# Kernel tuning notes

Measured on AMD Instinct MI355X. Metric: run time of the kernel, lower is better.

## Reference

```python
import jax, jax.numpy as jnp
import numpy as np

NEG_SLOPE = 0.01  # torch LeakyReLU default
VAR = 0.1


def _leaky(z):
    return jnp.where(z >= 0, z, NEG_SLOPE * z)


def _sconv(theta, bias, L, x):
    # theta: (C_out, C_in, 2), L: (M, M), x: (B, C_in, M)
    Lx = jnp.einsum('mn,bin->bim', L, x)                     # degree-1 Laplacian term
    y = jnp.einsum('oi,bim->bom', theta[:, :, 0], x) \
        + jnp.einsum('oi,bim->bom', theta[:, :, 1], Lx)
    if bias is not None:
        y = y + bias
    return y


def setup_inputs() -> dict:
    key = jax.random.key(0)
    ks = iter(jax.random.split(key, 32))
    B, Cin = 8, 4
    Ms = [2000, 6000, 4000]
    inp = {}
    for d, M in enumerate(Ms):
        inp[f'L{d}'] = jax.random.normal(next(ks), (M, M), jnp.float32) / np.sqrt(M)
        inp[f'x{d}'] = jax.random.normal(next(ks), (B, Cin, M), jnp.float32)
        inp[f'th{d}_1'] = VAR * jax.random.normal(next(ks), (16, 4, 2), jnp.float32)
        inp[f'b{d}_1'] = jnp.zeros((1, 16, 1), jnp.float32)
        inp[f'th{d}_2'] = VAR * jax.random.normal(next(ks), (32, 16, 2), jnp.float32)
    dims = [(96, 64), (64, 32), (32, 16), (16, 2)]
    for i, (din, dout) in enumerate(dims, start=1):
        bound = 1.0 / np.sqrt(din)
        inp[f'W{i}'] = jax.random.uniform(next(ks), (dout, din), jnp.float32, -bound, bound)
        inp[f'bb{i}'] = jax.random.uniform(next(ks), (dout,), jnp.float32, -bound, bound)
    return inp


def reference(L0, L1, L2, x0, x1, x2,
              th0_1, b0_1, th0_2,
              th1_1, b1_1, th1_2,
              th2_1, b2_1, th2_2,
              W1, bb1, W2, bb2, W3, bb3, W4, bb4):
    out0_1 = _sconv(th0_1, b0_1, L0, x0)
    out1_1 = _sconv(th1_1, b1_1, L1, x1)
    out2_1 = _sconv(th2_1, b2_1, L2, x2)
    out0_2 = _sconv(th0_2, None, L0, _leaky(out0_1))   # (B, 32, M0)
    out1_2 = _sconv(th1_2, None, L1, _leaky(out1_1))
    out2_2 = _sconv(th2_2, None, L2, _leaky(out2_1))
    # mean-pool over simplices, concat along channel dim -> (B, 96)
    pooled = jnp.concatenate([out0_2.mean(axis=2), out1_2.mean(axis=2), out2_2.mean(axis=2)], axis=1)
    h = pooled @ W1.T + bb1      # dropouts are identity at inference
    h = h @ W2.T + bb2
    h = h @ W3.T + bb3
    logits = h @ W4.T + bb4      # (B, 2)
    return (logits, out0_2, out1_2, out2_2)
```

## Files before the change

kernel.cpp:

```cpp
#include <hip/hip_runtime.h>
#include <stdint.h>

typedef __attribute__((ext_vector_type(4))) float f32x4;
typedef __attribute__((ext_vector_type(8))) __bf16 bf16x8;

constexpr int MS_[3] = {2000, 6000, 4000};
constexpr int MP_[3] = {2048, 6016, 4032};
constexpr int KS_[3] = {512, 1536, 1024};
constexpr int RB_[3] = {32, 94, 63};
constexpr int NB_[3] = {128, 376, 252};
constexpr int NTILE = 189;
constexpr int NGEMMB = 756;
constexpr long long OUT_OFF_[3] = {16, 512016, 2048016};

__device__ __forceinline__ unsigned short f2bf(float f) {
  __bf16 b = (__bf16)f;
  return *reinterpret_cast<unsigned short*>(&b);
}

__device__ __forceinline__ void gload_lds16(const void* g, void* l) {
  __builtin_amdgcn_global_load_lds(
      (const __attribute__((address_space(1))) unsigned int*)g,
      (__attribute__((address_space(3))) unsigned int*)l, 16, 0, 0);
}

__device__ __forceinline__ void tile_decode(int bid, int& d, int& t) {
  if (bid < RB_[0]) { d = 0; t = bid; }
  else if (bid < RB_[0] + RB_[1]) { d = 1; t = bid - RB_[0]; }
  else { d = 2; t = bid - RB_[0] - RB_[1]; }
}

struct PrepArgs {
  const float* x[3];
  unsigned short* xT[3];
  float* zero0; int zero_n;
};

__global__ __launch_bounds__(256) void prep_k(PrepArgs pa) {
  int d, t; tile_decode(blockIdx.x, d, t);
  const int M = MS_[d], Mp = MP_[d];
  const float* x = pa.x[d];
  unsigned short* xT = pa.xT[d];
  const int tid = threadIdx.x;
  const int m0 = t * 64;
  const int ml = tid & 63, cg = tid >> 6;
  const int m = m0 + ml;
  const bool valid = m < M;
#pragma unroll
  for (int it = 0; it < 8; ++it) {
    int c = it * 4 + cg;
    float v = valid ? x[(size_t)c * M + m] : 0.f;
    xT[(size_t)c * Mp + m] = f2bf(v);
  }
  if (blockIdx.x == 0) {
    for (int i = tid; i < pa.zero_n; i += 256) pa.zero0[i] = 0.f;
  }
}

struct GemmArgs {
  const float* L[3];
  const unsigned short* B[3];
  float* P[3];
};

template <int BN>
__global__ __launch_bounds__(256) void gemm_k(GemmArgs ga) {
  const int bid = blockIdx.x;
  int d, local;
  if (bid < NB_[0]) { d = 0; local = bid; }
  else if (bid < NB_[0] + NB_[1]) { d = 1; local = bid - NB_[0]; }
  else { d = 2; local = bid - NB_[0] - NB_[1]; }

  int M, Mp, KS, r, s;
  if (d == 0) { M = MS_[0]; Mp = MP_[0]; KS = KS_[0]; r = local & 31; s = local >> 5; }
  else if (d == 1) { M = MS_[1]; Mp = MP_[1]; KS = KS_[1]; r = local % 94; s = local / 94; }
  else { M = MS_[2]; Mp = MP_[2]; KS = KS_[2]; r = local % 63; s = local / 63; }

  const float* Lp = ga.L[d];
  const unsigned short* Bt = ga.B[d];
  float* Pp = ga.P[d];

  const int m0 = r * 64;
  const int kt0 = s * KS;
  const int nsteps = KS >> 6;

  __shared__ __align__(16) unsigned short Al[2][64 * 64];
  __shared__ __align__(16) unsigned short Bl[2][BN * 64];

  const int tid = threadIdx.x;
  const int lane = tid & 63;
  const int wave = tid >> 6;
  const int wr = wave >> 1, wc = wave & 1;
  constexpr int NR = BN / 32;

  f32x4 acc[2][NR];
#pragma unroll
  for (int a = 0; a < 2; ++a)
#pragma unroll
    for (int b = 0; b < NR; ++b) acc[a][b] = (f32x4){0.f, 0.f, 0.f, 0.f};

  auto stage = [&](int buf, int kt) {
#pragma unroll
    for (int l2 = 0; l2 < 2; ++l2) {
      int q = l2 * 256 + tid;
      int row = q >> 3;
      int col8 = (q & 7) * 8;
      int gm = m0 + row, gk = kt + col8;
      float4 v0 = make_float4(0.f, 0.f, 0.f, 0.f), v1 = v0;
      if (gm < M && gk < M) {
        const float* p = Lp + (size_t)gm * M + gk;
        v0 = *reinterpret_cast<const float4*>(p);
        v1 = *reinterpret_cast<const float4*>(p + 4);
      }
      union { unsigned short u[8]; int4 v; } pk;
      pk.u[0] = f2bf(v0.x); pk.u[1] = f2bf(v0.y); pk.u[2] = f2bf(v0.z); pk.u[3] = f2bf(v0.w);
      pk.u[4] = f2bf(v1.x); pk.u[5] = f2bf(v1.y); pk.u[6] = f2bf(v1.z); pk.u[7] = f2bf(v1.w);
      int idx = (row * 64 + col8) ^ ((row & 7) << 3);
      *reinterpret_cast<int4*>(&Al[buf][idx]) = pk.v;
    }
    int kb = (kt + 64 <= Mp) ? kt : (Mp - 64);
#pragma unroll
    for (int is = 0; is < BN / 32; ++is) {
      int c = is * 32 + (tid >> 3);
      int ke = ((tid & 7) * 8) ^ ((c & 7) << 3);
      gload_lds16(Bt + (size_t)c * Mp + kb + ke, &Bl[buf][is * 2048 + tid * 8]);
    }
  };

  auto compute = [&](int buf) {
    bf16x8 af[2][2];
    const int rA = wr * 32 + (lane & 15);
    const int kl = (lane >> 4) * 8;
#pragma unroll
    for (int mr = 0; mr < 2; ++mr)
#pragma unroll
      for (int kk = 0; kk < 2; ++kk) {
        int rr = rA + mr * 16;
        int idx = (rr * 64 + kk * 32 + kl) ^ ((rr & 7) << 3);
        af[mr][kk] = *reinterpret_cast<const bf16x8*>(&Al[buf][idx]);
      }
    bf16x8 bfr[NR][2];
    const int cB = wc * (BN / 2) + (lane & 15);
#pragma unroll
    for (int nr = 0; nr < NR; ++nr)
#pragma unroll
      for (int kk = 0; kk < 2; ++kk) {
        int cc = cB + nr * 16;
        int idx = (cc * 64 + kk * 32 + kl) ^ ((cc & 7) << 3);
        bfr[nr][kk] = *reinterpret_cast<const bf16x8*>(&Bl[buf][idx]);
      }
#pragma unroll
    for (int kk = 0; kk < 2; ++kk)
#pragma unroll
      for (int mr = 0; mr < 2; ++mr)
#pragma unroll
        for (int nr = 0; nr < NR; ++nr)
          acc[mr][nr] = __builtin_amdgcn_mfma_f32_16x16x32_bf16(
              af[mr][kk], bfr[nr][kk], acc[mr][nr], 0, 0, 0);
  };

  stage(0, kt0);
  for (int t = 0; t < nsteps; ++t) {
    __syncthreads();
    if (t + 1 < nsteps) stage((t + 1) & 1, kt0 + (t + 1) * 64);
    compute(t & 1);
  }

  const int colb = wc * (BN / 2) + (lane & 15);
  const int rowb = m0 + wr * 32 + ((lane >> 4) << 2);
#pragma unroll
  for (int mr = 0; mr < 2; ++mr)
#pragma unroll
    for (int nr = 0; nr < NR; ++nr)
#pragma unroll
      for (int j = 0; j < 4; ++j) {
        int rr = rowb + mr * 16 + j;
        int cc = colb + nr * 16;
        Pp[((size_t)s * Mp + rr) * BN + cc] = acc[mr][nr][j];
      }
}

struct EpiAArgs {
  const float* part1[3];
  const float* x[3];
  const float* th1[3];
  const float* b1[3];
  unsigned short* zT[3];
};

__global__ __launch_bounds__(256) void epiA_k(EpiAArgs ea) {
  int d, t; tile_decode(blockIdx.x, d, t);
  const int M = MS_[d], Mp = MP_[d];
  const int m0 = t * 64;
  __shared__ float Ys[32 * 66];
  __shared__ float Xs[32 * 66];
  const int tid = threadIdx.x;
  const float* part = ea.part1[d];
#pragma unroll
  for (int it = 0; it < 8; ++it) {
    int idx = it * 256 + tid;
    int m = idx >> 5, c = idx & 31;
    size_t base = (size_t)(m0 + m) * 32 + c;
    size_t st = (size_t)Mp * 32;
    float ssum = part[base] + part[st + base] + part[2 * st + base] + part[3 * st + base];
    Ys[c * 66 + m] = ssum;
  }
  {
    const float* x = ea.x[d];
    int m = tid & 63, cg = tid >> 6;
    bool valid = (m0 + m) < M;
#pragma unroll
    for (int it = 0; it < 8; ++it) {
      int c = it * 4 + cg;
      Xs[c * 66 + m] = valid ? x[(size_t)c * M + m0 + m] : 0.f;
    }
  }
  __syncthreads();
  const float* th = ea.th1[d];
  const float* bias = ea.b1[d];
  unsigned short* zT = ea.zT[d];
  const int m = tid & 63, cog = tid >> 6;
  const bool valid = (m0 + m) < M;
#pragma unroll
  for (int it = 0; it < 32; ++it) {
    int co = it * 4 + cog;
    int o = co & 15, b = co >> 4;
    float a = bias[o];
#pragma unroll
    for (int i = 0; i < 4; ++i) {
      int ci = b * 4 + i;
      a += th[(o * 4 + i) * 2] * Xs[ci * 66 + m] + th[(o * 4 + i) * 2 + 1] * Ys[ci * 66 + m];
    }
    float zz = (a >= 0.f) ? a : 0.01f * a;
    zT[(size_t)co * Mp + m0 + m] = valid ? f2bf(zz) : (unsigned short)0;
  }
}

struct EpiBArgs {
  const float* part2[3];
  const unsigned short* zT[3];
  const float* th2[3];
  float* out;
  float* csz;
  float* csy;
};

__global__ __launch_bounds__(256) void epiB_k(EpiBArgs eb) {
  int d, t; tile_decode(blockIdx.x, d, t);
  const int M = MS_[d], Mp = MP_[d];
  const int m0 = t * 64;
  __shared__ float Ys[128 * 66];
  __shared__ float red[256];
  const int tid = threadIdx.x;
  const float* part = eb.part2[d];
  float csum = 0.f;
#pragma unroll
  for (int it = 0; it < 32; ++it) {
    int idx = it * 256 + tid;
    int m = idx >> 7, c = idx & 127;
    size_t base = (size_t)(m0 + m) * 128 + c;
    size_t st = (size_t)Mp * 128;
    float ssum = part[base] + part[st + base] + part[2 * st + base] + part[3 * st + base];
    Ys[c * 66 + m] = ssum;
    csum += ssum;
  }
  red[tid] = csum;
  __syncthreads();
  if (tid < 128) atomicAdd(&eb.csy[d * 128 + tid], red[tid] + red[tid + 128]);

  const unsigned short* zT = eb.zT[d];
  const float* th = eb.th2[d];
  float* outp = eb.out + OUT_OFF_[d];
  const int m = tid & 63, g = tid >> 6;
  const bool valid = (m0 + m) < M;
#pragma unroll
  for (int bb = 0; bb < 2; ++bb) {
    int b = g * 2 + bb;
    float zv[16], yv[16];
#pragma unroll
    for (int o1 = 0; o1 < 16; ++o1) {
      int c = b * 16 + o1;
      unsigned short raw = zT[(size_t)c * Mp + m0 + m];
      __bf16 bf = *reinterpret_cast<__bf16*>(&raw);
      zv[o1] = (float)bf;
      yv[o1] = Ys[c * 66 + m];
    }
#pragma unroll
    for (int o1 = 0; o1 < 16; ++o1) {
      float v = zv[o1];
#pragma unroll
      for (int off = 32; off > 0; off >>= 1) v += __shfl_xor(v, off, 64);
      if (m == 0) atomicAdd(&eb.csz[d * 128 + b * 16 + o1], v);
    }
#pragma unroll
    for (int o2 = 0; o2 < 32; ++o2) {
      float v = 0.f;
#pragma unroll
      for (int o1 = 0; o1 < 16; ++o1)
        v += th[(o2 * 16 + o1) * 2] * zv[o1] + th[(o2 * 16 + o1) * 2 + 1] * yv[o1];
      if (valid) outp[(size_t)(b * 32 + o2) * M + m0 + m] = v;
    }
  }
}

struct MlpArgs {
  const float* csz; const float* csy;
  const float* th2[3];
  const float* W1; const float* b1;
  const float* W2; const float* b2;
  const float* W3; const float* b3;
  const float* W4; const float* b4;
  float* out;
};

__global__ __launch_bounds__(256) void mlp_k(MlpArgs ma) {
  __shared__ float pl[8][96];
  __shared__ float h1[8][64];
  __shared__ float h2[8][32];
  __shared__ float h3[8][16];
  const int tid = threadIdx.x;
  for (int id = tid; id < 768; id += 256) {
    int d = id >> 8, rem = id & 255, b = rem >> 5, o2 = rem & 31;
    const float* th = ma.th2[d];
    float invM = 1.f / (float)MS_[d];
    float v = 0.f;
    for (int o1 = 0; o1 < 16; ++o1)
      v += th[(o2 * 16 + o1) * 2] * ma.csz[d * 128 + b * 16 + o1] +
           th[(o2 * 16 + o1) * 2 + 1] * ma.csy[d * 128 + b * 16 + o1];
    pl[b][d * 32 + o2] = v * invM;
  }
  __syncthreads();
  for (int id = tid; id < 512; id += 256) {
    int b = id >> 6, j = id & 63;
    float v = ma.b1[j];
    for (int k = 0; k < 96; ++k) v += pl[b][k] * ma.W1[j * 96 + k];
    h1[b][j] = v;
  }
  __syncthreads();
  {
    int b = tid >> 5, j = tid & 31;
    float v = ma.b2[j];
    for (int k = 0; k < 64; ++k) v += h1[b][k] * ma.W2[j * 64 + k];
    h2[b][j] = v;
  }
  __syncthreads();
  if (tid < 128) {
    int b = tid >> 4, j = tid & 15;
    float v = ma.b3[j];
    for (int k = 0; k < 32; ++k) v += h2[b][k] * ma.W3[j * 32 + k];
    h3[b][j] = v;
  }
  __syncthreads();
  if (tid < 16) {
    int b = tid >> 1, j = tid & 1;
    float v = ma.b4[j];
    for (int k = 0; k < 16; ++k) v += h3[b][k] * ma.W4[j * 16 + k];
    ma.out[tid] = v;
  }
}

extern "C" void kernel_launch(void* const* d_in, const int* in_sizes, int n_in,
                              void* d_out, int out_size, void* d_ws, size_t ws_size,
                              hipStream_t stream) {
  (void)in_sizes; (void)n_in; (void)out_size; (void)ws_size;
  const float* L[3]   = {(const float*)d_in[0], (const float*)d_in[5], (const float*)d_in[10]};
  const float* x[3]   = {(const float*)d_in[1], (const float*)d_in[6], (const float*)d_in[11]};
  const float* th1[3] = {(const float*)d_in[2], (const float*)d_in[7], (const float*)d_in[12]};
  const float* b1[3]  = {(const float*)d_in[3], (const float*)d_in[8], (const float*)d_in[13]};
  const float* th2[3] = {(const float*)d_in[4], (const float*)d_in[9], (const float*)d_in[14]};
  const float* W1 = (const float*)d_in[15]; const float* bb1 = (const float*)d_in[16];
  const float* W2 = (const float*)d_in[17]; const float* bb2 = (const float*)d_in[18];
  const float* W3 = (const float*)d_in[19]; const float* bb3 = (const float*)d_in[20];
  const float* W4 = (const float*)d_in[21]; const float* bb4 = (const float*)d_in[22];
  float* out = (float*)d_out;

  char* ws = (char*)d_ws;
  size_t off = 0;
  auto alloc = [&](size_t bytes) {
    size_t r = off;
    off = (off + bytes + 255) & ~(size_t)255;
    return r;
  };
  const int MPs[3] = {2048, 6016, 4032};
  unsigned short* xT[3]; unsigned short* zT[3]; float* p1[3]; float* p2[3];
  for (int d = 0; d < 3; ++d) xT[d] = (unsigned short*)(ws + alloc((size_t)32 * MPs[d] * 2));
  for (int d = 0; d < 3; ++d) zT[d] = (unsigned short*)(ws + alloc((size_t)128 * MPs[d] * 2));
  for (int d = 0; d < 3; ++d) p1[d] = (float*)(ws + alloc((size_t)4 * MPs[d] * 32 * 4));
  for (int d = 0; d < 3; ++d) p2[d] = (float*)(ws + alloc((size_t)4 * MPs[d] * 128 * 4));
  float* csz = (float*)(ws + alloc((size_t)3 * 128 * 4));
  float* csy = (float*)(ws + alloc((size_t)3 * 128 * 4));

  PrepArgs pa;
  for (int d = 0; d < 3; ++d) { pa.x[d] = x[d]; pa.xT[d] = xT[d]; }
  pa.zero0 = csz; pa.zero_n = 768;
  prep_k<<<NTILE, 256, 0, stream>>>(pa);

  GemmArgs g1;
  for (int d = 0; d < 3; ++d) { g1.L[d] = L[d]; g1.B[d] = xT[d]; g1.P[d] = p1[d]; }
  gemm_k<32><<<NGEMMB, 256, 0, stream>>>(g1);

  EpiAArgs ea;
  for (int d = 0; d < 3; ++d) {
    ea.part1[d] = p1[d]; ea.x[d] = x[d]; ea.th1[d] = th1[d]; ea.b1[d] = b1[d]; ea.zT[d] = zT[d];
  }
  epiA_k<<<NTILE, 256, 0, stream>>>(ea);

  GemmArgs g2;
  for (int d = 0; d < 3; ++d) { g2.L[d] = L[d]; g2.B[d] = zT[d]; g2.P[d] = p2[d]; }
  gemm_k<128><<<NGEMMB, 256, 0, stream>>>(g2);

  EpiBArgs eb;
  for (int d = 0; d < 3; ++d) { eb.part2[d] = p2[d]; eb.zT[d] = zT[d]; eb.th2[d] = th2[d]; }
  eb.out = out; eb.csz = csz; eb.csy = csy;
  epiB_k<<<NTILE, 256, 0, stream>>>(eb);

  MlpArgs ma;
  ma.csz = csz; ma.csy = csy;
  for (int d = 0; d < 3; ++d) ma.th2[d] = th2[d];
  ma.W1 = W1; ma.b1 = bb1; ma.W2 = W2; ma.b2 = bb2;
  ma.W3 = W3; ma.b3 = bb3; ma.W4 = W4; ma.b4 = bb4;
  ma.out = out;
  mlp_k<<<1, 256, 0, stream>>>(ma);
}
```

Before: 190.3 us.

## Load GEMM operands directly into MFMA register fragments, dropping LDS staging

The GEMM kernel no longer stages L and the transposed activations through double-buffered shared memory with barriers. Each lane now loads its MFMA fragments straight from global memory into registers, converts the L values to bf16 in registers, and software-pipelines two register sets across k-steps. This removes LDS traffic and __syncthreads, but each wave now issues its own global loads with less coalescing, data is no longer shared across waves, and register pressure rises.

Result: slower. 251.7 us (+32.3%).

```diff
diff --git a/kernel.cpp b/kernel.cpp
--- a/kernel.cpp
+++ b/kernel.cpp
@@ -16,12 +16,6 @@
 __device__ __forceinline__ unsigned short f2bf(float f) {
   __bf16 b = (__bf16)f;
   return *reinterpret_cast<unsigned short*>(&b);
-}
-
-__device__ __forceinline__ void gload_lds16(const void* g, void* l) {
-  __builtin_amdgcn_global_load_lds(
-      (const __attribute__((address_space(1))) unsigned int*)g,
-      (__attribute__((address_space(3))) unsigned int*)l, 16, 0, 0);
 }
 
 __device__ __forceinline__ void tile_decode(int bid, int& d, int& t) {
@@ -76,22 +70,36 @@
   else if (d == 1) { M = MS_[1]; Mp = MP_[1]; KS = KS_[1]; r = local % 94; s = local / 94; }
   else { M = MS_[2]; Mp = MP_[2]; KS = KS_[2]; r = local % 63; s = local / 63; }
 
-  const float* Lp = ga.L[d];
-  const unsigned short* Bt = ga.B[d];
-  float* Pp = ga.P[d];
+  const float* __restrict__ Lp = ga.L[d];
+  const unsigned short* __restrict__ Bt = ga.B[d];
+  float* __restrict__ Pp = ga.P[d];
 
   const int m0 = r * 64;
   const int kt0 = s * KS;
   const int nsteps = KS >> 6;
-
-  __shared__ __align__(16) unsigned short Al[2][64 * 64];
-  __shared__ __align__(16) unsigned short Bl[2][BN * 64];
+  constexpr int NR = BN / 32;
 
   const int tid = threadIdx.x;
   const int lane = tid & 63;
   const int wave = tid >> 6;
   const int wr = wave >> 1, wc = wave & 1;
-  constexpr int NR = BN / 32;
+  const int lr = lane & 15;
+  const int kl = (lane >> 4) * 8;
+
+  const float* pA[2];
+  bool rok[2];
+#pragma unroll
+  for (int mr = 0; mr < 2; ++mr) {
+    int row = m0 + wr * 32 + mr * 16 + lr;
+    rok[mr] = row < M;
+    pA[mr] = Lp + (size_t)row * M;
+  }
+  const unsigned short* pB[NR];
+#pragma unroll
+  for (int nr = 0; nr < NR; ++nr) {
+    int c = wc * (BN / 2) + nr * 16 + lr;
+    pB[nr] = Bt + (size_t)c * Mp;
+  }
 
   f32x4 acc[2][NR];
 #pragma unroll
@@ -99,56 +107,37 @@
 #pragma unroll
     for (int b = 0; b < NR; ++b) acc[a][b] = (f32x4){0.f, 0.f, 0.f, 0.f};
 
-  auto stage = [&](int buf, int kt) {
-#pragma unroll
-    for (int l2 = 0; l2 < 2; ++l2) {
-      int q = l2 * 256 + tid;
-      int row = q >> 3;
-      int col8 = (q & 7) * 8;
-      int gm = m0 + row, gk = kt + col8;
-      float4 v0 = make_float4(0.f, 0.f, 0.f, 0.f), v1 = v0;
-      if (gm < M && gk < M) {
-        const float* p = Lp + (size_t)gm * M + gk;
-        v0 = *reinterpret_cast<const float4*>(p);
-        v1 = *reinterpret_cast<const float4*>(p + 4);
+  auto load = [&](f32x4 (&aS)[2][2][2], bf16x8 (&bS)[NR][2], int step) {
+    const int kb = kt0 + step * 64 + kl;
+#pragma unroll
+    for (int kk = 0; kk < 2; ++kk) {
+      const int k = kb + kk * 32;
+#pragma unroll
+      for (int mr = 0; mr < 2; ++mr) {
+        const bool ok = rok[mr] && (k + 8 <= M);
+        const f32x4 z = (f32x4){0.f, 0.f, 0.f, 0.f};
+        aS[mr][kk][0] = ok ? *reinterpret_cast<const f32x4*>(pA[mr] + k) : z;
+        aS[mr][kk][1] = ok ? *reinterpret_cast<const f32x4*>(pA[mr] + k + 4) : z;
       }
-      union { unsigned short u[8]; int4 v; } pk;
-      pk.u[0] = f2bf(v0.x); pk.u[1] = f2bf(v0.y); pk.u[2] = f2bf(v0.z); pk.u[3] = f2bf(v0.w);
-      pk.u[4] = f2bf(v1.x); pk.u[5] = f2bf(v1.y); pk.u[6] = f2bf(v1.z); pk.u[7] = f2bf(v1.w);
-      int idx = (row * 64 + col8) ^ ((row & 7) << 3);
-      *reinterpret_cast<int4*>(&Al[buf][idx]) = pk.v;
-    }
-    int kb = (kt + 64 <= Mp) ? kt : (Mp - 64);
-#pragma unroll
-    for (int is = 0; is < BN / 32; ++is) {
-      int c = is * 32 + (tid >> 3);
-      int ke = ((tid & 7) * 8) ^ ((c & 7) << 3);
-      gload_lds16(Bt + (size_t)c * Mp + kb + ke, &Bl[buf][is * 2048 + tid * 8]);
+      int kc = k;
+      if (kc > Mp - 8) kc = Mp - 8;
+#pragma unroll
+      for (int nr = 0; nr < NR; ++nr)
+        bS[nr][kk] = *reinterpret_cast<const bf16x8*>(pB[nr] + kc);
     }
   };
 
-  auto compute = [&](int buf) {
+  auto compute = [&](f32x4 (&aS)[2][2][2], bf16x8 (&bS)[NR][2]) {
     bf16x8 af[2][2];
-    const int rA = wr * 32 + (lane & 15);
-    const int kl = (lane >> 4) * 8;
 #pragma unroll
     for (int mr = 0; mr < 2; ++mr)
 #pragma unroll
-      for (int kk = 0; kk < 2; ++kk) {
-        int rr = rA + mr * 16;
-        int idx = (rr * 64 + kk * 32 + kl) ^ ((rr & 7) << 3);
-        af[mr][kk] = *reinterpret_cast<const bf16x8*>(&Al[buf][idx]);
-      }
-    bf16x8 bfr[NR][2];
-    const int cB = wc * (BN / 2) + (lane & 15);
-#pragma unroll
-    for (int nr = 0; nr < NR; ++nr)
-#pragma unroll
-      for (int kk = 0; kk < 2; ++kk) {
-        int cc = cB + nr * 16;
-        int idx = (cc * 64 + kk * 32 + kl) ^ ((cc & 7) << 3);
-        bfr[nr][kk] = *reinterpret_cast<const bf16x8*>(&Bl[buf][idx]);
-      }
+      for (int kk = 0; kk < 2; ++kk)
+#pragma unroll
+        for (int j = 0; j < 4; ++j) {
+          af[mr][kk][j] = (__bf16)aS[mr][kk][0][j];
+          af[mr][kk][4 + j] = (__bf16)aS[mr][kk][1][j];
+        }
 #pragma unroll
     for (int kk = 0; kk < 2; ++kk)
 #pragma unroll
@@ -156,17 +145,20 @@
 #pragma unroll
         for (int nr = 0; nr < NR; ++nr)
           acc[mr][nr] = __builtin_amdgcn_mfma_f32_16x16x32_bf16(
-              af[mr][kk], bfr[nr][kk], acc[mr][nr], 0, 0, 0);
+              af[mr][kk], bS[nr][kk], acc[mr][nr], 0, 0, 0);
   };
 
-  stage(0, kt0);
-  for (int t = 0; t < nsteps; ++t) {
-    __syncthreads();
-    if (t + 1 < nsteps) stage((t + 1) & 1, kt0 + (t + 1) * 64);
-    compute(t & 1);
-  }
-
-  const int colb = wc * (BN / 2) + (lane & 15);
+  f32x4 aP[2][2][2], aQ[2][2][2];
+  bf16x8 bP[NR][2], bQ[NR][2];
+  load(aP, bP, 0);
+  for (int t = 0; t < nsteps; t += 2) {
+    load(aQ, bQ, t + 1);
+    compute(aP, bP);
+    if (t + 2 < nsteps) load(aP, bP, t + 2);
+    compute(aQ, bQ);
+  }
+
+  const int colb = wc * (BN / 2) + lr;
   const int rowb = m0 + wr * 32 + ((lane >> 4) << 2);
 #pragma unroll
   for (int mr = 0; mr < 2; ++mr)
```
